# Kernel optimization log

Measured on AMD Instinct MI355X. Metric: run time of the kernel, lower is better.

## Reference

```python
import jax, jax.numpy as jnp
import numpy as np

B, S, D, L = 16, 512, 256, 8192
DROP_P = 0.2


def setup_inputs() -> dict:
    key = jax.random.key(0)
    k1, k2, k3 = jax.random.split(key, 3)
    x = jax.random.normal(k1, (B, S, D), dtype=jnp.float32)
    label_emb = jax.random.normal(k2, (B, L, D), dtype=jnp.float32)
    mask = jax.random.uniform(k3, (B, S)) < 0.9
    return {"x": x, "mask": mask, "label_emb": label_emb}


def reference(x, mask, label_emb):
    # scores = x @ label_emb^T : [B, S, L]
    scores = jnp.einsum("bsd,bld->bsl", x, label_emb)
    # softmax over label dim (last)
    probs = jax.nn.softmax(scores, axis=-1)
    # post-softmax token masking (non-standard order, faithful to original)
    probs = jnp.where(mask[:, :, None], probs, jnp.zeros((), probs.dtype))
    # dropout (training=True in original), deterministic key for reproducibility
    keep = jax.random.bernoulli(jax.random.key(42), 1.0 - DROP_P, probs.shape)
    probs = jnp.where(keep, probs / (1.0 - DROP_P), jnp.zeros((), probs.dtype))
    # attention pooling: scores^T @ x : [B, L, D]
    return jnp.einsum("bsl,bsd->bld", probs, x)
```

## Files before the change

kernel.cpp:

```cpp
#include <hip/hip_runtime.h>
#include <stdint.h>
#include <stddef.h>

#define B_ 16
#define S_ 512
#define D_ 256
#define L_ 8192

typedef unsigned short u16;
typedef _Float16 f16;
typedef f16 f16x4 __attribute__((ext_vector_type(4)));
typedef f16 f16x8 __attribute__((ext_vector_type(8)));
typedef float f32x4 __attribute__((ext_vector_type(4)));

__device__ __forceinline__ void gl16(const void* g, void* l) {
  __builtin_amdgcn_global_load_lds(
      (const __attribute__((address_space(1))) unsigned int*)g,
      (__attribute__((address_space(3))) unsigned int*)l, 16, 0, 0);
}

__device__ __forceinline__ uint32_t rotl32(uint32_t x, int r) {
  return (x << r) | (x >> (32 - r));
}
__device__ __forceinline__ bool drop_keep(uint32_t j) {
  const uint32_t k0 = 0u, k1 = 42u, k2 = 0x1BD11BDAu ^ k0 ^ k1;
  uint32_t v0 = 0u + k0;
  uint32_t v1 = j + k1;
#define TF_R(r) { v0 += v1; v1 = rotl32(v1, (r)); v1 ^= v0; }
  TF_R(13) TF_R(15) TF_R(26) TF_R(6)
  v0 += k1; v1 += k2 + 1u;
  TF_R(17) TF_R(29) TF_R(16) TF_R(24)
  v0 += k2; v1 += k0 + 2u;
  TF_R(13) TF_R(15) TF_R(26) TF_R(6)
  v0 += k0; v1 += k1 + 3u;
  TF_R(17) TF_R(29) TF_R(16) TF_R(24)
  v0 += k1; v1 += k2 + 4u;
  TF_R(13) TF_R(15) TF_R(26) TF_R(6)
  v0 += k2; v1 += k0 + 5u;
#undef TF_R
  uint32_t bits = v0 ^ v1;
  float u = __uint_as_float((bits >> 9) | 0x3f800000u) - 1.0f;
  return u < 0.8f;
}

__global__ __launch_bounds__(256)
void conv16_kernel(const float* __restrict__ src, f16* __restrict__ dst, int n) {
  int i = (blockIdx.x * 256 + threadIdx.x) * 8;
  if (i >= n) return;
  float4 a = *(const float4*)&src[i];
  float4 b = *(const float4*)&src[i + 4];
  f16x8 o;
  o[0] = (f16)a.x; o[1] = (f16)a.y; o[2] = (f16)a.z; o[3] = (f16)a.w;
  o[4] = (f16)b.x; o[5] = (f16)b.y; o[6] = (f16)b.z; o[7] = (f16)b.w;
  *(f16x8*)&dst[i] = o;
}

__global__ __launch_bounds__(256)
void xt16_kernel(const float* __restrict__ x, f16* __restrict__ xT) {
  const int b = blockIdx.z, sb = blockIdx.x * 32, db = blockIdx.y * 32;
  __shared__ float t[32][33];
  const int tid = threadIdx.x;
  const int r = tid >> 3, c4 = (tid & 7) * 4;
  float4 v = *(const float4*)&x[((size_t)b * S_ + sb + r) * D_ + db + c4];
  t[r][c4] = v.x; t[r][c4 + 1] = v.y; t[r][c4 + 2] = v.z; t[r][c4 + 3] = v.w;
  __syncthreads();
  const int dr = tid >> 3, s4 = (tid & 7) * 4;
  f16x4 o;
#pragma unroll
  for (int j = 0; j < 4; ++j) o[j] = (f16)t[s4 + j][dr];
  *(f16x4*)&xT[((size_t)b * D_ + db + dr) * S_ + sb + s4] = o;
}

__global__ __launch_bounds__(256)
void gemm1_f16(const f16* __restrict__ xh, const f16* __restrict__ eh,
               float* __restrict__ scores, float2* __restrict__ partials,
               int s0, int sc) {
  __shared__ __align__(16) f16 As[128 * 32];
  __shared__ __align__(16) f16 Bs[128 * 32];
  __shared__ float pmaxA[128][2];
  __shared__ float psumA[128][2];

  const int tid = threadIdx.x;
  const int lane = tid & 63, wave = tid >> 6;
  const int b = blockIdx.z, lt = blockIdx.x * 128, st = blockIdx.y * 128;

  const int ra = wave * 32 + (lane >> 2);
  const int kc = (lane & 3) * 8;
  const size_t offA0 = ((size_t)b * S_ + s0 + st + ra) * D_ + kc;
  const size_t offA1 = offA0 + 16 * D_;
  const size_t offB0 = ((size_t)b * L_ + lt + ra) * D_ + kc;
  const size_t offB1 = offB0 + 16 * D_;
  const int lo0 = wave * 2048 + lane * 16;

  const int lm = lane & 15, kq = lane >> 4;
  const int wm = (wave & 1) * 64, wn = (wave >> 1) * 64;

  f32x4 acc[4][4] = {};

  for (int k0 = 0; k0 < D_; k0 += 32) {
    __syncthreads();
    gl16(xh + offA0 + k0, (char*)As + lo0);
    gl16(xh + offA1 + k0, (char*)As + lo0 + 1024);
    gl16(eh + offB0 + k0, (char*)Bs + lo0);
    gl16(eh + offB1 + k0, (char*)Bs + lo0 + 1024);
    __syncthreads();

    f16x8 fa[4], fb[4];
#pragma unroll
    for (int mi = 0; mi < 4; ++mi)
      fa[mi] = *(const f16x8*)&As[(wm + mi * 16 + lm) * 32 + kq * 8];
#pragma unroll
    for (int ni = 0; ni < 4; ++ni)
      fb[ni] = *(const f16x8*)&Bs[(wn + ni * 16 + lm) * 32 + kq * 8];
#pragma unroll
    for (int mi = 0; mi < 4; ++mi)
#pragma unroll
      for (int ni = 0; ni < 4; ++ni)
        acc[mi][ni] = __builtin_amdgcn_mfma_f32_16x16x32_f16(
            fa[mi], fb[ni], acc[mi][ni], 0, 0, 0);
  }

#pragma unroll
  for (int mi = 0; mi < 4; ++mi)
#pragma unroll
    for (int ni = 0; ni < 4; ++ni) {
      const int m0 = wm + mi * 16 + kq * 4;
      const int n = wn + ni * 16 + lm;
      float* sp = scores + ((size_t)b * sc + st + m0) * L_ + lt + n;
#pragma unroll
      for (int r = 0; r < 4; ++r) sp[(size_t)r * L_] = acc[mi][ni][r];
    }

  float cmax[4][4];
#pragma unroll
  for (int mi = 0; mi < 4; ++mi)
#pragma unroll
    for (int r = 0; r < 4; ++r) {
      float v = acc[mi][0][r];
      v = fmaxf(v, acc[mi][1][r]);
      v = fmaxf(v, acc[mi][2][r]);
      cmax[mi][r] = fmaxf(v, acc[mi][3][r]);
    }
#pragma unroll
  for (int off = 1; off < 16; off <<= 1)
#pragma unroll
    for (int mi = 0; mi < 4; ++mi)
#pragma unroll
      for (int r = 0; r < 4; ++r)
        cmax[mi][r] = fmaxf(cmax[mi][r], __shfl_xor(cmax[mi][r], off, 64));
  if (lm == 0) {
#pragma unroll
    for (int mi = 0; mi < 4; ++mi)
#pragma unroll
      for (int r = 0; r < 4; ++r)
        pmaxA[wm + mi * 16 + kq * 4 + r][wave >> 1] = cmax[mi][r];
  }
  __syncthreads();
  float rowm[4][4];
#pragma unroll
  for (int mi = 0; mi < 4; ++mi)
#pragma unroll
    for (int r = 0; r < 4; ++r) {
      int row = wm + mi * 16 + kq * 4 + r;
      rowm[mi][r] = fmaxf(pmaxA[row][0], pmaxA[row][1]);
    }
  float psum[4][4] = {};
#pragma unroll
  for (int mi = 0; mi < 4; ++mi)
#pragma unroll
    for (int ni = 0; ni < 4; ++ni)
#pragma unroll
      for (int r = 0; r < 4; ++r)
        psum[mi][r] += __expf(acc[mi][ni][r] - rowm[mi][r]);
#pragma unroll
  for (int off = 1; off < 16; off <<= 1)
#pragma unroll
    for (int mi = 0; mi < 4; ++mi)
#pragma unroll
      for (int r = 0; r < 4; ++r)
        psum[mi][r] += __shfl_xor(psum[mi][r], off, 64);
  if (lm == 0) {
#pragma unroll
    for (int mi = 0; mi < 4; ++mi)
#pragma unroll
      for (int r = 0; r < 4; ++r)
        psumA[wm + mi * 16 + kq * 4 + r][wave >> 1] = psum[mi][r];
  }
  __syncthreads();
  if (tid < 128) {
    float m = fmaxf(pmaxA[tid][0], pmaxA[tid][1]);
    float Z = psumA[tid][0] + psumA[tid][1];
    partials[((size_t)b * 64 + blockIdx.x) * sc + st + tid] = make_float2(m, Z);
  }
}

__global__ __launch_bounds__(256)
void combine_kernel(const float2* __restrict__ partials,
                    const int* __restrict__ mask, float2* __restrict__ stats,
                    int s0, int sc) {
  const int idx = blockIdx.x * 256 + threadIdx.x;
  const int b = idx / sc, si = idx - b * sc;
  float m = -3.402823466e38f, Z = 0.f;
  for (int t = 0; t < 64; ++t) {
    float2 p = partials[((size_t)b * 64 + t) * sc + si];
    if (p.x > m) {
      Z = Z * __expf(m - p.x) + p.y;
      m = p.x;
    } else {
      Z += p.y * __expf(p.x - m);
    }
  }
  float f = (mask[b * S_ + s0 + si] != 0) ? (1.25f / Z) : 0.0f;
  stats[idx] = make_float2(m, f);
}

__global__ __launch_bounds__(512)
void gemm2_fused(const float* __restrict__ scores, const f16* __restrict__ xT,
                 const float2* __restrict__ stats, float* __restrict__ out) {
  __shared__ __align__(16) float Ss[32 * 128];
  __shared__ __align__(16) f16 Bs[256 * 32];
  __shared__ float2 stat_s[S_];

  const int tid = threadIdx.x;
  const int lane = tid & 63, wave = tid >> 6;
  const int b = blockIdx.z, lt = blockIdx.x * 128;

  stat_s[tid] = stats[b * S_ + tid];

  const int sw = wave & 3;
  const bool isB = wave >= 4;
  const size_t sc_base = (size_t)b * S_ * L_ + lt;
  const size_t xb_base = (size_t)b * D_ * S_;

  const int lm = lane & 15, kq = lane >> 4;
  const int l_loc = wave * 16 + lm;
  const uint32_t gbase =
      (uint32_t)(b * S_) * (uint32_t)L_ + (uint32_t)(lt + l_loc);

  f32x4 acc[16] = {};

  for (int k0 = 0; k0 < S_; k0 += 32) {
    __syncthreads();
    if (!isB) {
#pragma unroll
      for (int i = 0; i < 4; ++i) {
        const int c = sw * 4 + i;
        gl16(scores + sc_base + (size_t)(k0 + 2 * c + (lane >> 5)) * L_ +
                 (lane & 31) * 4,
             (char*)Ss + c * 1024);
      }
    } else {
#pragma unroll
      for (int i = 0; i < 4; ++i) {
        const int c = sw * 4 + i;
        gl16(xT + xb_base + (size_t)(c * 16 + (lane >> 2)) * S_ + k0 +
                 (lane & 3) * 8,
             (char*)Bs + c * 1024);
      }
    }
    __syncthreads();

    float pv[8];
#pragma unroll
    for (int j = 0; j < 8; ++j) {
      const int s_loc = kq * 8 + j;
      const float sc = Ss[s_loc * 128 + l_loc];
      const float2 mf = stat_s[k0 + s_loc];
      pv[j] = __expf(sc - mf.x) * mf.y;
    }
    f16x8 fa;
#pragma unroll
    for (int j = 0; j < 8; ++j) {
      const uint32_t gidx = gbase + (uint32_t)(k0 + kq * 8 + j) * (uint32_t)L_;
      fa[j] = drop_keep(gidx) ? (f16)pv[j] : (f16)0.f;
    }

#pragma unroll
    for (int ni = 0; ni < 16; ++ni) {
      const f16x8 fb = *(const f16x8*)&Bs[(ni * 16 + lm) * 32 + kq * 8];
      acc[ni] = __builtin_amdgcn_mfma_f32_16x16x32_f16(fa, fb, acc[ni], 0, 0, 0);
    }
  }

#pragma unroll
  for (int ni = 0; ni < 16; ++ni) {
    const int n = ni * 16 + lm;
    float* op = out + ((size_t)b * L_ + lt + wave * 16 + kq * 4) * D_ + n;
#pragma unroll
    for (int r = 0; r < 4; ++r) op[(size_t)r * D_] = acc[ni][r];
  }
}

extern "C" void kernel_launch(void* const* d_in, const int* in_sizes, int n_in,
                              void* d_out, int out_size, void* d_ws, size_t ws_size,
                              hipStream_t stream) {
  const float* x = (const float*)d_in[0];
  const int* mask = (const int*)d_in[1];
  const float* E = (const float*)d_in[2];
  float* out = (float*)d_out;

  char* ws = (char*)d_ws;
  const size_t nE = (size_t)B_ * L_ * D_;
  const size_t nX = (size_t)B_ * S_ * D_;
  size_t o = 0;
  f16* Eh = (f16*)(ws + o); o += nE * 2;
  f16* Xh = (f16*)(ws + o); o += nX * 2;
  f16* XT = (f16*)(ws + o); o += nX * 2;
  float2* stats = (float2*)(ws + o); o += (size_t)B_ * S_ * 8;
  float2* partials = (float2*)(ws + o); o += (size_t)B_ * 64 * S_ * 8;
  float* scores = (float*)(ws + o);

  conv16_kernel<<<dim3((unsigned)(nE / 8 / 256)), 256, 0, stream>>>(E, Eh, (int)nE);
  conv16_kernel<<<dim3((unsigned)(nX / 8 / 256)), 256, 0, stream>>>(x, Xh, (int)nX);
  xt16_kernel<<<dim3(S_ / 32, D_ / 32, B_), 256, 0, stream>>>(x, XT);

  gemm1_f16<<<dim3(L_ / 128, S_ / 128, B_), 256, 0, stream>>>(
      Xh, Eh, scores, partials, 0, S_);
  combine_kernel<<<dim3(B_ * S_ / 256), 256, 0, stream>>>(partials, mask,
                                                          stats, 0, S_);
  gemm2_fused<<<dim3(L_ / 128, 1, B_), 512, 0, stream>>>(scores, XT, stats, out);
}
```

Measured before the change: 542.0 us.

## Store scores transposed and double-buffer LDS staging in both GEMMs

The first GEMM now computes E·xᵀ, so scores are written in [L,S] order, and the softmax column statistics are reduced accordingly. Both GEMM kernels switch to double-buffered LDS tiles. The next tile's global-to-LDS load is issued before computing on the current one, which removes one barrier per iteration. The LDS layouts change to a k-chunk-major arrangement, and gemm2 now reads vectorized float4 score chunks. The cost is twice the shared memory, which may lower occupancy.

```diff
diff --git a/kernel.cpp b/kernel.cpp
--- a/kernel.cpp
+++ b/kernel.cpp
@@ -72,11 +72,10 @@
 }
 
 __global__ __launch_bounds__(256)
-void gemm1_f16(const f16* __restrict__ xh, const f16* __restrict__ eh,
-               float* __restrict__ scores, float2* __restrict__ partials,
-               int s0, int sc) {
-  __shared__ __align__(16) f16 As[128 * 32];
-  __shared__ __align__(16) f16 Bs[128 * 32];
+void gemm1t_f16(const f16* __restrict__ eh, const f16* __restrict__ xh,
+                float* __restrict__ scoresT, float2* __restrict__ partials) {
+  __shared__ __align__(16) f16 As[2][4096];
+  __shared__ __align__(16) f16 Bs[2][4096];
   __shared__ float pmaxA[128][2];
   __shared__ float psumA[128][2];
 
@@ -84,125 +83,115 @@
   const int lane = tid & 63, wave = tid >> 6;
   const int b = blockIdx.z, lt = blockIdx.x * 128, st = blockIdx.y * 128;
 
-  const int ra = wave * 32 + (lane >> 2);
-  const int kc = (lane & 3) * 8;
-  const size_t offA0 = ((size_t)b * S_ + s0 + st + ra) * D_ + kc;
-  const size_t offA1 = offA0 + 16 * D_;
-  const size_t offB0 = ((size_t)b * L_ + lt + ra) * D_ + kc;
-  const size_t offB1 = offB0 + 16 * D_;
-  const int lo0 = wave * 2048 + lane * 16;
-
   const int lm = lane & 15, kq = lane >> 4;
   const int wm = (wave & 1) * 64, wn = (wave >> 1) * 64;
 
+  const int c0 = wave * 2;
+  auto stage = [&](int bi, int k0) {
+#pragma unroll
+    for (int i = 0; i < 2; ++i) {
+      const int c = c0 + i, kqc = c >> 1, rb = (c & 1) * 64;
+      gl16(eh + ((size_t)b * L_ + lt + rb + lane) * D_ + k0 + kqc * 8,
+           (char*)As[bi] + c * 1024 + lane * 16);
+      gl16(xh + ((size_t)b * S_ + st + rb + lane) * D_ + k0 + kqc * 8,
+           (char*)Bs[bi] + c * 1024 + lane * 16);
+    }
+  };
+
   f32x4 acc[4][4] = {};
 
-  for (int k0 = 0; k0 < D_; k0 += 32) {
-    __syncthreads();
-    gl16(xh + offA0 + k0, (char*)As + lo0);
-    gl16(xh + offA1 + k0, (char*)As + lo0 + 1024);
-    gl16(eh + offB0 + k0, (char*)Bs + lo0);
-    gl16(eh + offB1 + k0, (char*)Bs + lo0 + 1024);
-    __syncthreads();
-
+  stage(0, 0);
+  __syncthreads();
+  int bi = 0;
+  for (int t = 0; t < 8; ++t) {
+    if (t < 7) stage(bi ^ 1, (t + 1) * 32);
     f16x8 fa[4], fb[4];
 #pragma unroll
     for (int mi = 0; mi < 4; ++mi)
-      fa[mi] = *(const f16x8*)&As[(wm + mi * 16 + lm) * 32 + kq * 8];
+      fa[mi] = *(const f16x8*)&As[bi][(kq * 128 + wm + mi * 16 + lm) * 8];
 #pragma unroll
     for (int ni = 0; ni < 4; ++ni)
-      fb[ni] = *(const f16x8*)&Bs[(wn + ni * 16 + lm) * 32 + kq * 8];
+      fb[ni] = *(const f16x8*)&Bs[bi][(kq * 128 + wn + ni * 16 + lm) * 8];
 #pragma unroll
     for (int mi = 0; mi < 4; ++mi)
 #pragma unroll
       for (int ni = 0; ni < 4; ++ni)
         acc[mi][ni] = __builtin_amdgcn_mfma_f32_16x16x32_f16(
             fa[mi], fb[ni], acc[mi][ni], 0, 0, 0);
+    __syncthreads();
+    bi ^= 1;
   }
 
 #pragma unroll
   for (int mi = 0; mi < 4; ++mi)
 #pragma unroll
     for (int ni = 0; ni < 4; ++ni) {
-      const int m0 = wm + mi * 16 + kq * 4;
-      const int n = wn + ni * 16 + lm;
-      float* sp = scores + ((size_t)b * sc + st + m0) * L_ + lt + n;
-#pragma unroll
-      for (int r = 0; r < 4; ++r) sp[(size_t)r * L_] = acc[mi][ni][r];
-    }
-
-  float cmax[4][4];
-#pragma unroll
-  for (int mi = 0; mi < 4; ++mi)
-#pragma unroll
-    for (int r = 0; r < 4; ++r) {
-      float v = acc[mi][0][r];
-      v = fmaxf(v, acc[mi][1][r]);
-      v = fmaxf(v, acc[mi][2][r]);
-      cmax[mi][r] = fmaxf(v, acc[mi][3][r]);
-    }
-#pragma unroll
-  for (int off = 1; off < 16; off <<= 1)
+      const int l0 = wm + mi * 16 + kq * 4;
+      const int s = wn + ni * 16 + lm;
+      float* sp = scoresT + ((size_t)b * L_ + lt + l0) * S_ + st + s;
+#pragma unroll
+      for (int r = 0; r < 4; ++r) sp[(size_t)r * S_] = acc[mi][ni][r];
+    }
+
+  float cmax[4];
+#pragma unroll
+  for (int ni = 0; ni < 4; ++ni) {
+    float v = acc[0][ni][0];
 #pragma unroll
     for (int mi = 0; mi < 4; ++mi)
 #pragma unroll
+      for (int r = 0; r < 4; ++r) v = fmaxf(v, acc[mi][ni][r]);
+    cmax[ni] = v;
+  }
+#pragma unroll
+  for (int ni = 0; ni < 4; ++ni) {
+    cmax[ni] = fmaxf(cmax[ni], __shfl_xor(cmax[ni], 16, 64));
+    cmax[ni] = fmaxf(cmax[ni], __shfl_xor(cmax[ni], 32, 64));
+  }
+  if (kq == 0) {
+#pragma unroll
+    for (int ni = 0; ni < 4; ++ni) pmaxA[wn + ni * 16 + lm][wave & 1] = cmax[ni];
+  }
+  __syncthreads();
+  float colm[4];
+#pragma unroll
+  for (int ni = 0; ni < 4; ++ni) {
+    const int s = wn + ni * 16 + lm;
+    colm[ni] = fmaxf(pmaxA[s][0], pmaxA[s][1]);
+  }
+  float psum[4] = {};
+#pragma unroll
+  for (int ni = 0; ni < 4; ++ni)
+#pragma unroll
+    for (int mi = 0; mi < 4; ++mi)
+#pragma unroll
       for (int r = 0; r < 4; ++r)
-        cmax[mi][r] = fmaxf(cmax[mi][r], __shfl_xor(cmax[mi][r], off, 64));
-  if (lm == 0) {
-#pragma unroll
-    for (int mi = 0; mi < 4; ++mi)
-#pragma unroll
-      for (int r = 0; r < 4; ++r)
-        pmaxA[wm + mi * 16 + kq * 4 + r][wave >> 1] = cmax[mi][r];
-  }
-  __syncthreads();
-  float rowm[4][4];
-#pragma unroll
-  for (int mi = 0; mi < 4; ++mi)
-#pragma unroll
-    for (int r = 0; r < 4; ++r) {
-      int row = wm + mi * 16 + kq * 4 + r;
-      rowm[mi][r] = fmaxf(pmaxA[row][0], pmaxA[row][1]);
-    }
-  float psum[4][4] = {};
-#pragma unroll
-  for (int mi = 0; mi < 4; ++mi)
-#pragma unroll
-    for (int ni = 0; ni < 4; ++ni)
-#pragma unroll
-      for (int r = 0; r < 4; ++r)
-        psum[mi][r] += __expf(acc[mi][ni][r] - rowm[mi][r]);
-#pragma unroll
-  for (int off = 1; off < 16; off <<= 1)
-#pragma unroll
-    for (int mi = 0; mi < 4; ++mi)
-#pragma unroll
-      for (int r = 0; r < 4; ++r)
-        psum[mi][r] += __shfl_xor(psum[mi][r], off, 64);
-  if (lm == 0) {
-#pragma unroll
-    for (int mi = 0; mi < 4; ++mi)
-#pragma unroll
-      for (int r = 0; r < 4; ++r)
-        psumA[wm + mi * 16 + kq * 4 + r][wave >> 1] = psum[mi][r];
+        psum[ni] += __expf(acc[mi][ni][r] - colm[ni]);
+#pragma unroll
+  for (int ni = 0; ni < 4; ++ni) {
+    psum[ni] += __shfl_xor(psum[ni], 16, 64);
+    psum[ni] += __shfl_xor(psum[ni], 32, 64);
+  }
+  if (kq == 0) {
+#pragma unroll
+    for (int ni = 0; ni < 4; ++ni) psumA[wn + ni * 16 + lm][wave & 1] = psum[ni];
   }
   __syncthreads();
   if (tid < 128) {
     float m = fmaxf(pmaxA[tid][0], pmaxA[tid][1]);
     float Z = psumA[tid][0] + psumA[tid][1];
-    partials[((size_t)b * 64 + blockIdx.x) * sc + st + tid] = make_float2(m, Z);
+    partials[((size_t)b * 64 + blockIdx.x) * S_ + st + tid] = make_float2(m, Z);
   }
 }
 
 __global__ __launch_bounds__(256)
 void combine_kernel(const float2* __restrict__ partials,
-                    const int* __restrict__ mask, float2* __restrict__ stats,
-                    int s0, int sc) {
+                    const int* __restrict__ mask, float2* __restrict__ stats) {
   const int idx = blockIdx.x * 256 + threadIdx.x;
-  const int b = idx / sc, si = idx - b * sc;
+  const int b = idx / S_, si = idx - b * S_;
   float m = -3.402823466e38f, Z = 0.f;
   for (int t = 0; t < 64; ++t) {
-    float2 p = partials[((size_t)b * 64 + t) * sc + si];
+    float2 p = partials[((size_t)b * 64 + t) * S_ + si];
     if (p.x > m) {
       Z = Z * __expf(m - p.x) + p.y;
       m = p.x;
@@ -210,15 +199,15 @@
       Z += p.y * __expf(p.x - m);
     }
   }
-  float f = (mask[b * S_ + s0 + si] != 0) ? (1.25f / Z) : 0.0f;
+  float f = (mask[idx] != 0) ? (1.25f / Z) : 0.0f;
   stats[idx] = make_float2(m, f);
 }
 
 __global__ __launch_bounds__(512)
-void gemm2_fused(const float* __restrict__ scores, const f16* __restrict__ xT,
+void gemm2_fused(const float* __restrict__ scoresT, const f16* __restrict__ xT,
                  const float2* __restrict__ stats, float* __restrict__ out) {
-  __shared__ __align__(16) float Ss[32 * 128];
-  __shared__ __align__(16) f16 Bs[256 * 32];
+  __shared__ __align__(16) float Ss[2][4096];
+  __shared__ __align__(16) f16 Bs[2][8192];
   __shared__ float2 stat_s[S_];
 
   const int tid = threadIdx.x;
@@ -226,47 +215,50 @@
   const int b = blockIdx.z, lt = blockIdx.x * 128;
 
   stat_s[tid] = stats[b * S_ + tid];
-
-  const int sw = wave & 3;
-  const bool isB = wave >= 4;
-  const size_t sc_base = (size_t)b * S_ * L_ + lt;
-  const size_t xb_base = (size_t)b * D_ * S_;
 
   const int lm = lane & 15, kq = lane >> 4;
   const int l_loc = wave * 16 + lm;
   const uint32_t gbase =
       (uint32_t)(b * S_) * (uint32_t)L_ + (uint32_t)(lt + l_loc);
 
+  const int c0 = wave * 2;
+  auto stage = [&](int bi, int k0) {
+#pragma unroll
+    for (int i = 0; i < 2; ++i) {
+      const int c = c0 + i;
+      {
+        const int gs = c >> 1, lb = (c & 1) * 64;
+        gl16(scoresT + ((size_t)b * L_ + lt + lb + lane) * S_ + k0 + gs * 4,
+             (char*)Ss[bi] + c * 1024 + lane * 16);
+      }
+      {
+        const int kqc = c >> 2, db = (c & 3) * 64;
+        gl16(xT + ((size_t)b * D_ + db + lane) * S_ + k0 + kqc * 8,
+             (char*)Bs[bi] + c * 1024 + lane * 16);
+      }
+    }
+  };
+
   f32x4 acc[16] = {};
 
+  stage(0, 0);
+  __syncthreads();
+  int bi = 0;
   for (int k0 = 0; k0 < S_; k0 += 32) {
-    __syncthreads();
-    if (!isB) {
-#pragma unroll
-      for (int i = 0; i < 4; ++i) {
-        const int c = sw * 4 + i;
-        gl16(scores + sc_base + (size_t)(k0 + 2 * c + (lane >> 5)) * L_ +
-                 (lane & 31) * 4,
-             (char*)Ss + c * 1024);
-      }
-    } else {
-#pragma unroll
-      for (int i = 0; i < 4; ++i) {
-        const int c = sw * 4 + i;
-        gl16(xT + xb_base + (size_t)(c * 16 + (lane >> 2)) * S_ + k0 +
-                 (lane & 3) * 8,
-             (char*)Bs + c * 1024);
-      }
-    }
-    __syncthreads();
-
+    if (k0 < S_ - 32) stage(bi ^ 1, k0 + 32);
+
+    const f32x4 v0 = *(const f32x4*)&Ss[bi][((kq * 2 + 0) * 128 + l_loc) * 4];
+    const f32x4 v1 = *(const f32x4*)&Ss[bi][((kq * 2 + 1) * 128 + l_loc) * 4];
     float pv[8];
 #pragma unroll
-    for (int j = 0; j < 8; ++j) {
-      const int s_loc = kq * 8 + j;
-      const float sc = Ss[s_loc * 128 + l_loc];
-      const float2 mf = stat_s[k0 + s_loc];
-      pv[j] = __expf(sc - mf.x) * mf.y;
+    for (int j = 0; j < 4; ++j) {
+      const float2 mf = stat_s[k0 + kq * 8 + j];
+      pv[j] = __expf(v0[j] - mf.x) * mf.y;
+    }
+#pragma unroll
+    for (int j = 0; j < 4; ++j) {
+      const float2 mf = stat_s[k0 + kq * 8 + 4 + j];
+      pv[4 + j] = __expf(v1[j] - mf.x) * mf.y;
     }
     f16x8 fa;
 #pragma unroll
@@ -277,9 +269,11 @@
 
 #pragma unroll
     for (int ni = 0; ni < 16; ++ni) {
-      const f16x8 fb = *(const f16x8*)&Bs[(ni * 16 + lm) * 32 + kq * 8];
+      const f16x8 fb = *(const f16x8*)&Bs[bi][(kq * 256 + ni * 16 + lm) * 8];
       acc[ni] = __builtin_amdgcn_mfma_f32_16x16x32_f16(fa, fb, acc[ni], 0, 0, 0);
     }
+    __syncthreads();
+    bi ^= 1;
   }
 
 #pragma unroll
@@ -308,15 +302,14 @@
   f16* XT = (f16*)(ws + o); o += nX * 2;
   float2* stats = (float2*)(ws + o); o += (size_t)B_ * S_ * 8;
   float2* partials = (float2*)(ws + o); o += (size_t)B_ * 64 * S_ * 8;
-  float* scores = (float*)(ws + o);
+  float* scoresT = (float*)(ws + o);
 
   conv16_kernel<<<dim3((unsigned)(nE / 8 / 256)), 256, 0, stream>>>(E, Eh, (int)nE);
   conv16_kernel<<<dim3((unsigned)(nX / 8 / 256)), 256, 0, stream>>>(x, Xh, (int)nX);
   xt16_kernel<<<dim3(S_ / 32, D_ / 32, B_), 256, 0, stream>>>(x, XT);
 
-  gemm1_f16<<<dim3(L_ / 128, S_ / 128, B_), 256, 0, stream>>>(
-      Xh, Eh, scores, partials, 0, S_);
-  combine_kernel<<<dim3(B_ * S_ / 256), 256, 0, stream>>>(partials, mask,
-                                                          stats, 0, S_);
-  gemm2_fused<<<dim3(L_ / 128, 1, B_), 512, 0, stream>>>(scores, XT, stats, out);
-}
+  gemm1t_f16<<<dim3(L_ / 128, S_ / 128, B_), 256, 0, stream>>>(
+      Eh, Xh, scoresT, partials);
+  combine_kernel<<<dim3(B_ * S_ / 256), 256, 0, stream>>>(partials, mask, stats);
+  gemm2_fused<<<dim3(L_ / 128, 1, B_), 512, 0, stream>>>(scoresT, XT, stats, out);
+}
```

Result: slower. 612.1 us (+12.9%).
